# Performance work log

Hardware: AMD Instinct MI355X
Metric: run time of the kernel (lower is better)

## Reference

```python
import jax, jax.numpy as jnp
import numpy as np

B, D_IN, H = 8192, 4096, 128
E, N, C = 3, 256, 32          # experts, codebook_size, codebook_dim
D1, D2 = 512, 256             # down_units
U1, U2 = 256, 512             # up_units
CW = 0.25                     # commitment_weight


def setup_inputs() -> dict:
    key = jax.random.key(0)
    ks = jax.random.split(key, 16)
    s = 0.02
    f32 = jnp.float32
    inp = {
        'x':   jax.random.normal(ks[0], (B, D_IN), f32),
        # llm_down MLP: 4096 -> 512 -> 256 -> 128 (ReLU on hiddens, linear out)
        'Wd1': jax.random.normal(ks[1], (D_IN, D1), f32) * s, 'bd1': jnp.zeros((D1,), f32),
        'Wd2': jax.random.normal(ks[2], (D1, D2), f32) * s,  'bd2': jnp.zeros((D2,), f32),
        'Wd3': jax.random.normal(ks[3], (D2, H), f32) * s,   'bd3': jnp.zeros((H,), f32),
        # per-expert VQ: project_in 128->32, codebook [256,32], project_out 32->128
        'Win':  jax.random.normal(ks[4], (E, H, C), f32) * s, 'bin_': jnp.zeros((E, C), f32),
        'codebook': jax.random.normal(ks[5], (E, N, C), f32),
        'Wout': jax.random.normal(ks[6], (E, C, H), f32) * s, 'bout': jnp.zeros((E, H), f32),
        # llm_up MLP: 128 -> 256 -> 512 -> 4096
        'Wu1': jax.random.normal(ks[7], (H, U1), f32) * s,   'bu1': jnp.zeros((U1,), f32),
        'Wu2': jax.random.normal(ks[8], (U1, U2), f32) * s,  'bu2': jnp.zeros((U2,), f32),
        'Wu3': jax.random.normal(ks[9], (U2, D_IN), f32) * s, 'bu3': jnp.zeros((D_IN,), f32),
    }
    return inp


def _decorrelation_loss(qemb):
    # qemb: [B, E, H]
    b, e, h = qemb.shape
    cen = qemb - qemb.mean(axis=0, keepdims=True)
    cen = cen.transpose(1, 0, 2).reshape(e, -1)          # [E, B*H]
    cov = (cen @ cen.T) / (b * h - 1)                    # [E, E]
    std = jnp.sqrt(jnp.diag(cov))
    std = jnp.where(std > 1e-8, std, 1.0)
    corr = cov / jnp.outer(std, std)
    c2 = corr ** 2
    return c2.sum() - jnp.diag(c2).sum()


def _vq_experts(latent, Win, bin_, codebook, Wout, bout):
    # latent: [B,H]; all experts share the same (unmasked) latent.
    xe = jnp.einsum('bh,ehc->ebc', latent, Win) + bin_[:, None, :]      # [E,B,C]
    d2 = ((xe ** 2).sum(-1)[..., None]
          - 2.0 * jnp.einsum('ebc,enc->ebn', xe, codebook)
          + (codebook ** 2).sum(-1)[:, None, :])                        # [E,B,N]
    idx = jnp.argmin(d2, axis=-1)                                       # [E,B]
    q = jax.vmap(lambda c, i: c[i])(codebook, idx)                      # [E,B,C] gather
    commit = CW * jnp.mean((jax.lax.stop_gradient(q) - xe) ** 2, axis=(1, 2)).sum()
    quant = xe + jax.lax.stop_gradient(q - xe)                          # straight-through
    qe = jnp.einsum('ebc,ech->ebh', quant, Wout) + bout[:, None, :]     # [E,B,H]
    return qe, idx, commit


def reference(x, Wd1, bd1, Wd2, bd2, Wd3, bd3, Win, bin_, codebook, Wout, bout,
              Wu1, bu1, Wu2, bu2, Wu3, bu3):
    h = jax.nn.relu(x @ Wd1 + bd1)
    h = jax.nn.relu(h @ Wd2 + bd2)
    latent = h @ Wd3 + bd3                                              # [B,128]
    qe, idx, total_commit = _vq_experts(latent, Win, bin_, codebook, Wout, bout)
    qemb = qe.transpose(1, 0, 2)                                        # [B,E,H]
    decorr = _decorrelation_loss(qemb)
    rl = qemb.mean(axis=1)                                              # [B,H]
    u = jax.nn.relu(rl @ Wu1 + bu1)
    u = jax.nn.relu(u @ Wu2 + bu2)
    recon = jnp.clip(u @ Wu3 + bu3, -1.0, 1.0)                          # [B,4096]
    return (recon, idx.T, total_commit, decorr)
```

## Files before the change

kernel.cpp:

```cpp
#include <hip/hip_runtime.h>
#include <hip/hip_bf16.h>

using bf16 = __hip_bfloat16;

typedef __bf16 bf16x8 __attribute__((ext_vector_type(8)));
typedef float  f32x4  __attribute__((ext_vector_type(4)));
typedef unsigned int u32x4 __attribute__((ext_vector_type(4)));
typedef unsigned long long u64;
typedef unsigned short u16;
typedef unsigned int u32;

__device__ __forceinline__ float b2f(bf16 v) { return __bfloat162float(v); }
__device__ __forceinline__ bf16  f2b(float v) { return __float2bfloat16(v); }
__device__ __forceinline__ u16   bits(bf16 v) { return __builtin_bit_cast(u16, v); }

static constexpr size_t SZ_WD1S = 512ull  * 8192  * 2;
static constexpr size_t SZ_WD2S = 256ull  * 1536  * 2;
static constexpr size_t SZ_WFUS = 128ull  * 768   * 2;
static constexpr size_t SZ_WU1T = 256ull  * 128   * 2;
static constexpr size_t SZ_WU2T = 512ull  * 256   * 2;
static constexpr size_t SZ_WU3T = 4096ull * 512   * 2;
static constexpr size_t SZ_H1S  = 8192ull * 1536  * 2;
static constexpr size_t SZ_H2S  = 8192ull * 768   * 2;
static constexpr size_t SZ_XE   = 8192ull * 128   * 4;
static constexpr size_t SZ_QEMB = 3ull * 8192 * 128 * 4;
static constexpr size_t SZ_RL   = 8192ull * 128   * 2;
static constexpr size_t SZ_U1   = 8192ull * 256   * 2;
static constexpr size_t SZ_U2   = 8192ull * 512   * 2;
static constexpr size_t SZ_CNRM = 768ull * 4;
static constexpr size_t SZ_BFUS = 128ull * 4;
static constexpr size_t SZ_PART = 4ull * 8192 * 512 * 4;

static constexpr size_t OFF_WD1S = 0;
static constexpr size_t OFF_WD2S = OFF_WD1S + SZ_WD1S;
static constexpr size_t OFF_WFUS = OFF_WD2S + SZ_WD2S;
static constexpr size_t OFF_WU1T = OFF_WFUS + SZ_WFUS;
static constexpr size_t OFF_WU2T = OFF_WU1T + SZ_WU1T;
static constexpr size_t OFF_WU3T = OFF_WU2T + SZ_WU2T;
static constexpr size_t OFF_H1S  = OFF_WU3T + SZ_WU3T;
static constexpr size_t OFF_H2S  = OFF_H1S  + SZ_H1S;
static constexpr size_t OFF_XE   = OFF_H2S  + SZ_H2S;
static constexpr size_t OFF_QEMB = OFF_XE   + SZ_XE;
static constexpr size_t OFF_RL   = OFF_QEMB + SZ_QEMB;
static constexpr size_t OFF_U1   = OFF_RL   + SZ_RL;
static constexpr size_t OFF_U2   = OFF_U1   + SZ_U1;
static constexpr size_t OFF_CNRM = OFF_U2   + SZ_U2;
static constexpr size_t OFF_BFUS = OFF_CNRM + ((SZ_CNRM + 255) & ~size_t(255));
static constexpr size_t OFF_STAT = OFF_BFUS + ((SZ_BFUS + 255) & ~size_t(255));
static constexpr size_t OFF_PART = OFF_STAT + 2048;

__global__ void wtrans_bf16(const float* __restrict__ in, bf16* __restrict__ out,
                            int K, int N)
{
    __shared__ float tile[32][33];
    const int tx = threadIdx.x, ty = threadIdx.y;
    const int n0 = blockIdx.x * 32, k0 = blockIdx.y * 32;
    #pragma unroll
    for (int i = 0; i < 32; i += 8)
        tile[ty + i][tx] = in[(size_t)(k0 + ty + i) * N + n0 + tx];
    __syncthreads();
    #pragma unroll
    for (int i = 0; i < 32; i += 8)
        out[(size_t)(n0 + ty + i) * K + k0 + tx] = f2b(tile[tx][ty + i]);
}

__global__ void wtrans_split3(const float* __restrict__ in, bf16* __restrict__ out,
                              int K, int N)
{
    __shared__ float tile[32][33];
    const int tx = threadIdx.x, ty = threadIdx.y;
    const int n0 = blockIdx.x * 32, k0 = blockIdx.y * 32;
    #pragma unroll
    for (int i = 0; i < 32; i += 8)
        tile[ty + i][tx] = in[(size_t)(k0 + ty + i) * N + n0 + tx];
    __syncthreads();
    #pragma unroll
    for (int i = 0; i < 32; i += 8) {
        const float v = tile[tx][ty + i];
        const bf16 hi = f2b(v);
        const bf16 lo = f2b(v - b2f(hi));
        bf16* o = out + (size_t)(n0 + ty + i) * 3 * K + 3 * (k0 + tx);
        o[0] = hi; o[1] = lo; o[2] = hi;
    }
}

__global__ void wtrans_hilo(const float* __restrict__ in, bf16* __restrict__ out,
                            int K, int N)
{
    __shared__ float tile[32][33];
    const int tx = threadIdx.x, ty = threadIdx.y;
    const int n0 = blockIdx.x * 32, k0 = blockIdx.y * 32;
    #pragma unroll
    for (int i = 0; i < 32; i += 8)
        tile[ty + i][tx] = in[(size_t)(k0 + ty + i) * N + n0 + tx];
    __syncthreads();
    const int kg = k0 >> 5;
    #pragma unroll
    for (int i = 0; i < 32; i += 8) {
        const float v = tile[tx][ty + i];
        const bf16 hi = f2b(v);
        const bf16 lo = f2b(v - b2f(hi));
        bf16* o = out + (size_t)(n0 + ty + i) * 8192 + kg * 64 + tx;
        o[0] = hi; o[32] = lo;
    }
}

__global__ void cnorm_kernel(const float* __restrict__ cb, float* __restrict__ cnorm)
{
    const int i = blockIdx.x * blockDim.x + threadIdx.x;
    if (i < 768) {
        float s = 0.f;
        for (int k = 0; k < 32; ++k) { const float v = cb[i * 32 + k]; s += v * v; }
        cnorm[i] = s;
    }
}

__global__ __launch_bounds__(256)
void wfuse_kernel(const float* __restrict__ Wd3, const float* __restrict__ bd3,
                  const float* __restrict__ Win, const float* __restrict__ bin_,
                  bf16* __restrict__ BtS, float* __restrict__ bfuse)
{
    const int n = blockIdx.x;
    const int t = threadIdx.x;
    if (n >= 96) {
        bf16* o = BtS + (size_t)n * 768 + 3 * t;
        o[0] = f2b(0.f); o[1] = f2b(0.f); o[2] = f2b(0.f);
        if (t == 0) bfuse[n] = 0.f;
        return;
    }
    const int e = n >> 5, c = n & 31;
    float s = 0.f;
    for (int h = 0; h < 128; ++h)
        s += Wd3[t * 128 + h] * Win[(size_t)(e * 128 + h) * 32 + c];
    const bf16 hi = f2b(s);
    const bf16 lo = f2b(s - b2f(hi));
    bf16* o = BtS + (size_t)n * 768 + 3 * t;
    o[0] = hi; o[1] = lo; o[2] = hi;
    if (t == 0) {
        float b = bin_[e * 32 + c];
        for (int h = 0; h < 128; ++h)
            b += bd3[h] * Win[(size_t)(e * 128 + h) * 32 + c];
        bfuse[n] = b;
    }
}

__global__ __launch_bounds__(256, 4)
void gemm1_x3(const float* __restrict__ A, const bf16* __restrict__ Bhl,
              float* __restrict__ part)
{
    __shared__ bf16 As[128 * 64];
    __shared__ bf16 Bs[128 * 64];
    const int t = threadIdx.x, lane = t & 63, w = t >> 6;
    const int n0 = blockIdx.x * 128;
    const int m0 = blockIdx.y * 128;
    const int kz = blockIdx.z;
    const int wr = w >> 1, wc = w & 1, l15 = lane & 15, quad = lane >> 4;
    const int offh = ((quad ^ (l15 & 7)) << 3);
    const int offl = offh ^ 32;

    f32x4 acc[4][4];
    #pragma unroll
    for (int i = 0; i < 4; ++i)
        #pragma unroll
        for (int j = 0; j < 4; ++j)
            #pragma unroll
            for (int r = 0; r < 4; ++r) acc[i][j][r] = 0.f;

    const int arow = t >> 1, ahalf = t & 1, arx = arow & 7;
    bf16* const aw0 = As + arow * 64 + (((ahalf * 2 + 0) ^ arx) << 3);
    bf16* const aw1 = As + arow * 64 + (((ahalf * 2 + 1) ^ arx) << 3);
    bf16* const aw2 = As + arow * 64 + (((4 + ahalf * 2 + 0) ^ arx) << 3);
    bf16* const aw3 = As + arow * 64 + (((4 + ahalf * 2 + 1) ^ arx) << 3);

    int brow[4], bco[4];
    #pragma unroll
    for (int i = 0; i < 4; ++i) {
        const int p = i * 256 + t;
        brow[i] = p >> 3;
        bco[i] = ((p & 7) ^ (brow[i] & 7)) * 8;
    }

    const int s0 = kz * 32, s1 = s0 + 32;
    for (int ks = s0; ks < s1; ++ks) {
        const float* ap = A + (size_t)(m0 + arow) * 4096 + ks * 32 + ahalf * 16;
        float f[16];
        *(float4*)(f + 0)  = *(const float4*)(ap + 0);
        *(float4*)(f + 4)  = *(const float4*)(ap + 4);
        *(float4*)(f + 8)  = *(const float4*)(ap + 8);
        *(float4*)(f + 12) = *(const float4*)(ap + 12);
        #pragma unroll
        for (int i = 0; i < 4; ++i) {
            const bf16* gb = Bhl + (size_t)(n0 + brow[i]) * 8192 + ks * 64 + bco[i];
            __builtin_amdgcn_global_load_lds(
                (const __attribute__((address_space(1))) void*)gb,
                (__attribute__((address_space(3))) void*)(Bs + (size_t)(i * 256 + t) * 8), 16, 0, 0);
        }
        {
            u32x4 hv, lv;
            #pragma unroll
            for (int j = 0; j < 4; ++j) {
                const bf16 h0 = f2b(f[2 * j]), h1 = f2b(f[2 * j + 1]);
                const u32 l0 = bits(f2b(f[2 * j] - b2f(h0)));
                const u32 l1 = bits(f2b(f[2 * j + 1] - b2f(h1)));
                hv[j] = (u32)bits(h0) | ((u32)bits(h1) << 16);
                lv[j] = l0 | (l1 << 16);
            }
            *(u32x4*)aw0 = hv; *(u32x4*)aw2 = lv;
            #pragma unroll
            for (int j = 0; j < 4; ++j) {
                const bf16 h0 = f2b(f[8 + 2 * j]), h1 = f2b(f[8 + 2 * j + 1]);
                const u32 l0 = bits(f2b(f[8 + 2 * j] - b2f(h0)));
                const u32 l1 = bits(f2b(f[8 + 2 * j + 1] - b2f(h1)));
                hv[j] = (u32)bits(h0) | ((u32)bits(h1) << 16);
                lv[j] = l0 | (l1 << 16);
            }
            *(u32x4*)aw1 = hv; *(u32x4*)aw3 = lv;
        }
        __syncthreads();
        {
            bf16x8 ah[4], al[4];
            #pragma unroll
            for (int mi = 0; mi < 4; ++mi) {
                const bf16* ar = As + (wr * 64 + mi * 16 + l15) * 64;
                ah[mi] = *(const bf16x8*)(ar + offh);
                al[mi] = *(const bf16x8*)(ar + offl);
            }
            #pragma unroll
            for (int ni = 0; ni < 4; ++ni) {
                const bf16* br = Bs + (wc * 64 + ni * 16 + l15) * 64;
                const bf16x8 bh = *(const bf16x8*)(br + offh);
                const bf16x8 bl = *(const bf16x8*)(br + offl);
                #pragma unroll
                for (int mi = 0; mi < 4; ++mi) {
                    acc[mi][ni] = __builtin_amdgcn_mfma_f32_16x16x32_bf16(ah[mi], bh, acc[mi][ni], 0, 0, 0);
                    acc[mi][ni] = __builtin_amdgcn_mfma_f32_16x16x32_bf16(al[mi], bh, acc[mi][ni], 0, 0, 0);
                    acc[mi][ni] = __builtin_amdgcn_mfma_f32_16x16x32_bf16(ah[mi], bl, acc[mi][ni], 0, 0, 0);
                }
            }
        }
        __syncthreads();
    }

    float* op = part + (size_t)kz * (8192ull * 512);
    #pragma unroll
    for (int mi = 0; mi < 4; ++mi)
        #pragma unroll
        for (int ni = 0; ni < 4; ++ni) {
            const int col = n0 + wc * 64 + ni * 16 + l15;
            #pragma unroll
            for (int r = 0; r < 4; ++r) {
                const int row = m0 + wr * 64 + mi * 16 + quad * 4 + r;
                op[(size_t)row * 512 + col] = acc[mi][ni][r];
            }
        }
}

__global__ __launch_bounds__(256)
void h1_epi(const float* __restrict__ part, const float* __restrict__ bias,
            bf16* __restrict__ out)
{
    const int idx = blockIdx.x * 256 + threadIdx.x;
    const int r = idx >> 7, c4 = idx & 127;
    const size_t base = (size_t)r * 512 + c4 * 4;
    const float4 p0 = *(const float4*)(part + 0ull * 8192 * 512 + base);
    const float4 p1 = *(const float4*)(part + 1ull * 8192 * 512 + base);
    const float4 p2 = *(const float4*)(part + 2ull * 8192 * 512 + base);
    const float4 p3 = *(const float4*)(part + 3ull * 8192 * 512 + base);
    const float4 bv = *(const float4*)(bias + c4 * 4);
    float v[4];
    v[0] = p0.x + p1.x + p2.x + p3.x + bv.x;
    v[1] = p0.y + p1.y + p2.y + p3.y + bv.y;
    v[2] = p0.z + p1.z + p2.z + p3.z + bv.z;
    v[3] = p0.w + p1.w + p2.w + p3.w + bv.w;
    u64 h[4], l[4];
    #pragma unroll
    for (int j = 0; j < 4; ++j) {
        const float vv = v[j] > 0.f ? v[j] : 0.f;
        const bf16 hi = f2b(vv);
        h[j] = bits(hi);
        l[j] = bits(f2b(vv - b2f(hi)));
    }
    const u64 w0 = h[0] | (h[0] << 16) | (l[0] << 32) | (h[1] << 48);
    const u64 w1 = h[1] | (l[1] << 16) | (h[2] << 32) | (h[2] << 48);
    const u64 w2 = l[2] | (h[3] << 16) | (h[3] << 32) | (l[3] << 48);
    u64* dst = (u64*)(out + (size_t)r * 1536 + 12 * c4);
    dst[0] = w0; dst[1] = w1; dst[2] = w2;
}

template <int EPI, int RELU>
__global__ __launch_bounds__(256)
void gemm_bt(const bf16* __restrict__ A, const bf16* __restrict__ Bt,
             const float* __restrict__ bias, void* __restrict__ outp,
             int M, int N, int K)
{
    __shared__ bf16 As[128 * 64];
    __shared__ bf16 Bs[128 * 64];
    const int t = threadIdx.x, lane = t & 63, w = t >> 6;
    const int n0 = blockIdx.x * 128;
    const int m0 = blockIdx.y * 128;
    const int wr = w >> 1, wc = w & 1, l15 = lane & 15, quad = lane >> 4;
    const int l7 = l15 & 7;

    f32x4 acc[4][4];
    #pragma unroll
    for (int i = 0; i < 4; ++i)
        #pragma unroll
        for (int j = 0; j < 4; ++j)
            #pragma unroll
            for (int r = 0; r < 4; ++r) acc[i][j][r] = 0.f;

    int lrow[4], lcol[4];
    #pragma unroll
    for (int i = 0; i < 4; ++i) {
        const int c = i * 256 + t;
        lrow[i] = c >> 3;
        lcol[i] = ((c & 7) ^ (lrow[i] & 7)) * 8;
    }

    for (int k0 = 0; k0 < K; k0 += 64) {
        #pragma unroll
        for (int i = 0; i < 4; ++i) {
            const int c = i * 256 + t;
            const bf16* ga = A  + (size_t)(m0 + lrow[i]) * K + k0 + lcol[i];
            const bf16* gb = Bt + (size_t)(n0 + lrow[i]) * K + k0 + lcol[i];
            __builtin_amdgcn_global_load_lds(
                (const __attribute__((address_space(1))) void*)ga,
                (__attribute__((address_space(3))) void*)(As + (size_t)c * 8), 16, 0, 0);
            __builtin_amdgcn_global_load_lds(
                (const __attribute__((address_space(1))) void*)gb,
                (__attribute__((address_space(3))) void*)(Bs + (size_t)c * 8), 16, 0, 0);
        }
        __syncthreads();
        #pragma unroll
        for (int kk = 0; kk < 2; ++kk) {
            const int sw = (((kk << 2) | quad) ^ l7) << 3;
            bf16x8 af[4], bfr[4];
            #pragma unroll
            for (int mi = 0; mi < 4; ++mi)
                af[mi] = *(const bf16x8*)(As + (wr * 64 + mi * 16 + l15) * 64 + sw);
            #pragma unroll
            for (int ni = 0; ni < 4; ++ni)
                bfr[ni] = *(const bf16x8*)(Bs + (wc * 64 + ni * 16 + l15) * 64 + sw);
            #pragma unroll
            for (int mi = 0; mi < 4; ++mi)
                #pragma unroll
                for (int ni = 0; ni < 4; ++ni)
                    acc[mi][ni] = __builtin_amdgcn_mfma_f32_16x16x32_bf16(
                        af[mi], bfr[ni], acc[mi][ni], 0, 0, 0);
        }
        __syncthreads();
    }

    #pragma unroll
    for (int mi = 0; mi < 4; ++mi)
        #pragma unroll
        for (int ni = 0; ni < 4; ++ni) {
            const int col = n0 + wc * 64 + ni * 16 + l15;
            const float bv = bias[col];
            #pragma unroll
            for (int r = 0; r < 4; ++r) {
                const int row = m0 + wr * 64 + mi * 16 + quad * 4 + r;
                float v = acc[mi][ni][r] + bv;
                if (RELU) v = v > 0.f ? v : 0.f;
                if (EPI == 0) {
                    ((float*)outp)[(size_t)row * N + col] = v;
                } else if (EPI == 1) {
                    const bf16 hi = f2b(v);
                    const bf16 lo = f2b(v - b2f(hi));
                    bf16* o = (bf16*)outp + (size_t)row * 3 * N + 3 * col;
                    o[0] = hi; o[1] = hi; o[2] = lo;
                } else if (EPI == 2) {
                    ((bf16*)outp)[(size_t)row * N + col] = f2b(v);
                } else {
                    v = fminf(fmaxf(v, -1.f), 1.f);
                    ((float*)outp)[(size_t)row * N + col] = v;
                }
            }
        }
}

__global__ __launch_bounds__(256)
void vq2_kernel(const float* __restrict__ xe_buf, const float* __restrict__ cb,
                const float* __restrict__ cnorm, const float* __restrict__ Wout,
                const float* __restrict__ bout, float* __restrict__ qemb,
                float* __restrict__ idx_out, float* __restrict__ commit_acc)
{
    __shared__ float cb_s[256 * 36];
    __shared__ float wo_s[32 * 128];
    __shared__ float cn_s[256];
    __shared__ float bo_s[128];
    __shared__ float xe_s[4 * 32];
    __shared__ float q_s[4 * 32];
    __shared__ int   idx_s[4];
    __shared__ u64   wred[4][4];
    __shared__ float cred[256];

    const int e  = blockIdx.x >> 6;
    const int rb = blockIdx.x & 63;
    const int t = threadIdx.x, lane = t & 63, w = t >> 6;

    for (int j = t; j < 256 * 32; j += 256) {
        const int code = j >> 5, c = j & 31;
        cb_s[code * 36 + c] = cb[(size_t)e * 8192 + j];
    }
    for (int j = t; j < 4096; j += 256) wo_s[j] = Wout[(size_t)e * 4096 + j];
    cn_s[t] = cnorm[e * 256 + t];
    if (t < 128) bo_s[t] = bout[e * 128 + t];
    float commit_loc = 0.f;
    __syncthreads();

    for (int it = 0; it < 32; ++it) {
        const int r0 = rb * 128 + it * 4;
        if (t < 128) {
            const int r4 = t >> 5, c = t & 31;
            xe_s[r4 * 32 + c] = xe_buf[(size_t)(r0 + r4) * 128 + e * 32 + c];
        }
        __syncthreads();

        u64 key[4];
        {
            const float4* cp = (const float4*)(cb_s + t * 36);
            const float cn = cn_s[t];
            #pragma unroll
            for (int r4 = 0; r4 < 4; ++r4) {
                float dot = 0.f;
                #pragma unroll
                for (int c4 = 0; c4 < 8; ++c4) {
                    const float4 cv = cp[c4];
                    const float4 xv = *(const float4*)(xe_s + r4 * 32 + c4 * 4);
                    dot += xv.x * cv.x + xv.y * cv.y + xv.z * cv.z + xv.w * cv.w;
                }
                const float d = cn - 2.f * dot;
                u32 ub = __builtin_bit_cast(u32, d);
                ub = (ub & 0x80000000u) ? ~ub : (ub | 0x80000000u);
                key[r4] = ((u64)ub << 32) | (u32)t;
            }
        }
        #pragma unroll
        for (int off = 32; off; off >>= 1) {
            #pragma unroll
            for (int r4 = 0; r4 < 4; ++r4) {
                const u64 o = __shfl_down(key[r4], off, 64);
                if (o < key[r4]) key[r4] = o;
            }
        }
        if (lane == 0) {
            #pragma unroll
            for (int r4 = 0; r4 < 4; ++r4) wred[r4][w] = key[r4];
        }
        __syncthreads();
        if (t < 4) {
            u64 k = wred[t][0];
            #pragma unroll
            for (int ww = 1; ww < 4; ++ww) if (wred[t][ww] < k) k = wred[t][ww];
            const int code = (int)(k & 0xFFFFFFFFu);
            idx_s[t] = code;
            idx_out[(size_t)(r0 + t) * 3 + e] = (float)code;
        }
        __syncthreads();
        if (t < 128) {
            const int r4 = t >> 5, c = t & 31;
            const float q = cb_s[idx_s[r4] * 36 + c];
            q_s[r4 * 32 + c] = q;
            const float dd = q - xe_s[r4 * 32 + c];
            commit_loc += dd * dd;
        }
        __syncthreads();
        #pragma unroll
        for (int p = 0; p < 2; ++p) {
            const int j = p * 256 + t;
            const int r4 = j >> 7, h = j & 127;
            float s = bo_s[h];
            #pragma unroll
            for (int c = 0; c < 32; ++c) s += q_s[r4 * 32 + c] * wo_s[c * 128 + h];
            qemb[((size_t)e * 8192 + r0 + r4) * 128 + h] = s;
        }
        __syncthreads();
    }

    cred[t] = commit_loc;
    __syncthreads();
    for (int o = 128; o; o >>= 1) { if (t < o) cred[t] += cred[t + o]; __syncthreads(); }
    if (t == 0) atomicAdd(commit_acc, cred[0]);
}

__global__ __launch_bounds__(256)
void rlmean_kernel(const float* __restrict__ qemb, bf16* __restrict__ rl,
                   float* __restrict__ meanAcc)
{
    const int t = threadIdx.x, h = t & 127, half = t >> 7;
    const int r0 = blockIdx.x * 64;
    float a0 = 0.f, a1 = 0.f, a2 = 0.f;
    for (int r = r0 + half; r < r0 + 64; r += 2) {
        const float v0 = qemb[((size_t)0 * 8192 + r) * 128 + h];
        const float v1 = qemb[((size_t)1 * 8192 + r) * 128 + h];
        const float v2 = qemb[((size_t)2 * 8192 + r) * 128 + h];
        a0 += v0; a1 += v1; a2 += v2;
        rl[(size_t)r * 128 + h] = f2b((v0 + v1 + v2) * (1.f / 3.f));
    }
    __shared__ float red[3][256];
    red[0][t] = a0; red[1][t] = a1; red[2][t] = a2;
    __syncthreads();
    if (t < 128) {
        atomicAdd(&meanAcc[0 * 128 + h], red[0][t] + red[0][t + 128]);
        atomicAdd(&meanAcc[1 * 128 + h], red[1][t] + red[1][t + 128]);
        atomicAdd(&meanAcc[2 * 128 + h], red[2][t] + red[2][t + 128]);
    }
}

__global__ __launch_bounds__(256)
void gram_kernel(const float* __restrict__ qemb, const float* __restrict__ meanAcc,
                 double* __restrict__ gram)
{
    const int t = threadIdx.x;
    const int h = t & 127, half = t >> 7;
    const int b0 = blockIdx.x * 32;
    const float m0 = meanAcc[0 * 128 + h] * (1.f / 8192.f);
    const float m1 = meanAcc[1 * 128 + h] * (1.f / 8192.f);
    const float m2 = meanAcc[2 * 128 + h] * (1.f / 8192.f);
    float g[6] = {0, 0, 0, 0, 0, 0};
    for (int b = b0 + half; b < b0 + 32; b += 2) {
        const float v0 = qemb[((size_t)0 * 8192 + b) * 128 + h] - m0;
        const float v1 = qemb[((size_t)1 * 8192 + b) * 128 + h] - m1;
        const float v2 = qemb[((size_t)2 * 8192 + b) * 128 + h] - m2;
        g[0] += v0 * v0; g[1] += v0 * v1; g[2] += v0 * v2;
        g[3] += v1 * v1; g[4] += v1 * v2; g[5] += v2 * v2;
    }
    __shared__ float red[256];
    for (int i = 0; i < 6; ++i) {
        red[t] = g[i];
        __syncthreads();
        for (int o = 128; o; o >>= 1) { if (t < o) red[t] += red[t + o]; __syncthreads(); }
        if (t == 0) atomicAdd(&gram[i], (double)red[0]);
        __syncthreads();
    }
}

__global__ void final_kernel(const float* __restrict__ commit_acc,
                             const double* __restrict__ gram,
                             float* __restrict__ out2)
{
    if (threadIdx.x != 0 || blockIdx.x != 0) return;
    const double denom = 8192.0 * 128.0 - 1.0;
    const double c00 = gram[0] / denom, c01 = gram[1] / denom, c02 = gram[2] / denom;
    const double c11 = gram[3] / denom, c12 = gram[4] / denom, c22 = gram[5] / denom;
    double s0 = sqrt(c00), s1 = sqrt(c11), s2 = sqrt(c22);
    if (!(s0 > 1e-8)) s0 = 1.0;
    if (!(s1 > 1e-8)) s1 = 1.0;
    if (!(s2 > 1e-8)) s2 = 1.0;
    const double r01 = c01 / (s0 * s1), r02 = c02 / (s0 * s2), r12 = c12 / (s1 * s2);
    const double decorr = 2.0 * (r01 * r01 + r02 * r02 + r12 * r12);
    out2[0] = (float)((double)commit_acc[0] * (0.25 / (8192.0 * 32.0)));
    out2[1] = (float)decorr;
}

extern "C" void kernel_launch(void* const* d_in, const int* in_sizes, int n_in,
                              void* d_out, int out_size, void* d_ws, size_t ws_size,
                              hipStream_t stream)
{
    const float* x    = (const float*)d_in[0];
    const float* Wd1  = (const float*)d_in[1];
    const float* bd1  = (const float*)d_in[2];
    const float* Wd2  = (const float*)d_in[3];
    const float* bd2  = (const float*)d_in[4];
    const float* Wd3  = (const float*)d_in[5];
    const float* bd3  = (const float*)d_in[6];
    const float* Win  = (const float*)d_in[7];
    const float* bin_ = (const float*)d_in[8];
    const float* cb   = (const float*)d_in[9];
    const float* Wout = (const float*)d_in[10];
    const float* bout = (const float*)d_in[11];
    const float* Wu1  = (const float*)d_in[12];
    const float* bu1  = (const float*)d_in[13];
    const float* Wu2  = (const float*)d_in[14];
    const float* bu2  = (const float*)d_in[15];
    const float* Wu3  = (const float*)d_in[16];
    const float* bu3  = (const float*)d_in[17];

    char* ws = (char*)d_ws;
    bf16*  Wd1s   = (bf16*)(ws + OFF_WD1S);
    bf16*  Wd2s   = (bf16*)(ws + OFF_WD2S);
    bf16*  WfuseS = (bf16*)(ws + OFF_WFUS);
    bf16*  Wu1T   = (bf16*)(ws + OFF_WU1T);
    bf16*  Wu2T   = (bf16*)(ws + OFF_WU2T);
    bf16*  Wu3T   = (bf16*)(ws + OFF_WU3T);
    bf16*  h1s    = (bf16*)(ws + OFF_H1S);
    bf16*  h2s    = (bf16*)(ws + OFF_H2S);
    float* xe     = (float*)(ws + OFF_XE);
    float* qemb   = (float*)(ws + OFF_QEMB);
    bf16*  rl     = (bf16*)(ws + OFF_RL);
    bf16*  u1     = (bf16*)(ws + OFF_U1);
    bf16*  u2     = (bf16*)(ws + OFF_U2);
    float* cnorm  = (float*)(ws + OFF_CNRM);
    float* bfuse  = (float*)(ws + OFF_BFUS);
    float* commit = (float*)(ws + OFF_STAT);
    double* gram  = (double*)(ws + OFF_STAT + 8);
    float* meanA  = (float*)(ws + OFF_STAT + 64);
    float* part   = (float*)(ws + OFF_PART);

    float* out_f   = (float*)d_out;
    float* idx_out = out_f + (size_t)8192 * 4096;
    float* scal    = idx_out + (size_t)8192 * 3;

    hipMemsetAsync(ws + OFF_STAT, 0, 2048, stream);

    const dim3 tb(32, 8);
    wtrans_hilo<<<dim3(16, 128), tb, 0, stream>>>(Wd1, Wd1s, 4096, 512);
    wtrans_split3<<<dim3(8, 16),   tb, 0, stream>>>(Wd2, Wd2s, 512, 256);
    wtrans_bf16<<<dim3(8, 4),      tb, 0, stream>>>(Wu1, Wu1T, 128, 256);
    wtrans_bf16<<<dim3(16, 8),     tb, 0, stream>>>(Wu2, Wu2T, 256, 512);
    wtrans_bf16<<<dim3(128, 16),   tb, 0, stream>>>(Wu3, Wu3T, 512, 4096);
    cnorm_kernel<<<3, 256, 0, stream>>>(cb, cnorm);
    wfuse_kernel<<<128, 256, 0, stream>>>(Wd3, bd3, Win, bin_, WfuseS, bfuse);

    gemm1_x3<<<dim3(4, 64, 4), 256, 0, stream>>>(x, Wd1s, part);
    h1_epi<<<4096, 256, 0, stream>>>(part, bd1, h1s);
    gemm_bt<1, 1><<<dim3(2, 64), 256, 0, stream>>>(h1s, Wd2s, bd2, h2s, 8192, 256, 1536);
    gemm_bt<0, 0><<<dim3(1, 64), 256, 0, stream>>>(h2s, WfuseS, bfuse, xe, 8192, 128, 768);

    vq2_kernel<<<192, 256, 0, stream>>>(xe, cb, cnorm, Wout, bout, qemb, idx_out, commit);
    rlmean_kernel<<<128, 256, 0, stream>>>(qemb, rl, meanA);
    gram_kernel<<<256, 256, 0, stream>>>(qemb, meanA, gram);
    final_kernel<<<1, 64, 0, stream>>>(commit, gram, scal);

    gemm_bt<2, 1><<<dim3(2, 64),  256, 0, stream>>>(rl, Wu1T, bu1, u1,    8192, 256,  128);
    gemm_bt<2, 1><<<dim3(4, 64),  256, 0, stream>>>(u1, Wu2T, bu2, u2,    8192, 512,  256);
    gemm_bt<3, 0><<<dim3(32, 64), 256, 0, stream>>>(u2, Wu3T, bu3, out_f, 8192, 4096, 512);

    (void)in_sizes; (void)n_in; (void)out_size; (void)ws_size;
}
```

Measured before the change: 627.0 us.

## Remap gemm1 blocks per XCD and split VQ kernel into more blocks

The first GEMM's block index is remapped so that blocks landing on the same XCD (bid & 7) share the same N/K weight panel, which should improve L2 reuse of the B operand across the chiplets. Separately, the VQ kernel launches 768 blocks of 32 rows each instead of 192 blocks of 128 rows, so more CUs stay busy. The cost is that each VQ block reloads the codebook and Wout into shared memory over fewer rows, which raises redundant global traffic.

Measured after the change: 586.8 us. 1.07x faster.

```diff
diff --git a/kernel.cpp b/kernel.cpp
--- a/kernel.cpp
+++ b/kernel.cpp
@@ -151,9 +151,12 @@
     __shared__ bf16 As[128 * 64];
     __shared__ bf16 Bs[128 * 64];
     const int t = threadIdx.x, lane = t & 63, w = t >> 6;
-    const int n0 = blockIdx.x * 128;
-    const int m0 = blockIdx.y * 128;
-    const int kz = blockIdx.z;
+    const int bid = blockIdx.x + blockIdx.y * 4 + blockIdx.z * 256;
+    const int xcd = bid & 7, j = bid >> 3;
+    const int panel = xcd + 8 * (j >> 6);
+    const int n0 = (panel & 3) * 128;
+    const int kz = panel >> 2;
+    const int m0 = (j & 63) * 128;
     const int wr = w >> 1, wc = w & 1, l15 = lane & 15, quad = lane >> 4;
     const int offh = ((quad ^ (l15 & 7)) << 3);
     const int offl = offh ^ 32;
@@ -162,9 +165,9 @@
     #pragma unroll
     for (int i = 0; i < 4; ++i)
         #pragma unroll
-        for (int j = 0; j < 4; ++j)
-            #pragma unroll
-            for (int r = 0; r < 4; ++r) acc[i][j][r] = 0.f;
+        for (int jj = 0; jj < 4; ++jj)
+            #pragma unroll
+            for (int r = 0; r < 4; ++r) acc[i][jj][r] = 0.f;
 
     const int arow = t >> 1, ahalf = t & 1, arx = arow & 7;
     bf16* const aw0 = As + arow * 64 + (((ahalf * 2 + 0) ^ arx) << 3);
@@ -198,21 +201,21 @@
         {
             u32x4 hv, lv;
             #pragma unroll
-            for (int j = 0; j < 4; ++j) {
-                const bf16 h0 = f2b(f[2 * j]), h1 = f2b(f[2 * j + 1]);
-                const u32 l0 = bits(f2b(f[2 * j] - b2f(h0)));
-                const u32 l1 = bits(f2b(f[2 * j + 1] - b2f(h1)));
-                hv[j] = (u32)bits(h0) | ((u32)bits(h1) << 16);
-                lv[j] = l0 | (l1 << 16);
+            for (int jj = 0; jj < 4; ++jj) {
+                const bf16 h0 = f2b(f[2 * jj]), h1 = f2b(f[2 * jj + 1]);
+                const u32 l0 = bits(f2b(f[2 * jj] - b2f(h0)));
+                const u32 l1 = bits(f2b(f[2 * jj + 1] - b2f(h1)));
+                hv[jj] = (u32)bits(h0) | ((u32)bits(h1) << 16);
+                lv[jj] = l0 | (l1 << 16);
             }
             *(u32x4*)aw0 = hv; *(u32x4*)aw2 = lv;
             #pragma unroll
-            for (int j = 0; j < 4; ++j) {
-                const bf16 h0 = f2b(f[8 + 2 * j]), h1 = f2b(f[8 + 2 * j + 1]);
-                const u32 l0 = bits(f2b(f[8 + 2 * j] - b2f(h0)));
-                const u32 l1 = bits(f2b(f[8 + 2 * j + 1] - b2f(h1)));
-                hv[j] = (u32)bits(h0) | ((u32)bits(h1) << 16);
-                lv[j] = l0 | (l1 << 16);
+            for (int jj = 0; jj < 4; ++jj) {
+                const bf16 h0 = f2b(f[8 + 2 * jj]), h1 = f2b(f[8 + 2 * jj + 1]);
+                const u32 l0 = bits(f2b(f[8 + 2 * jj] - b2f(h0)));
+                const u32 l1 = bits(f2b(f[8 + 2 * jj + 1] - b2f(h1)));
+                hv[jj] = (u32)bits(h0) | ((u32)bits(h1) << 16);
+                lv[jj] = l0 | (l1 << 16);
             }
             *(u32x4*)aw1 = hv; *(u32x4*)aw3 = lv;
         }
@@ -395,8 +398,8 @@
     __shared__ u64   wred[4][4];
     __shared__ float cred[256];
 
-    const int e  = blockIdx.x >> 6;
-    const int rb = blockIdx.x & 63;
+    const int e  = blockIdx.x >> 8;
+    const int rb = blockIdx.x & 255;
     const int t = threadIdx.x, lane = t & 63, w = t >> 6;
 
     for (int j = t; j < 256 * 32; j += 256) {
@@ -409,8 +412,8 @@
     float commit_loc = 0.f;
     __syncthreads();
 
-    for (int it = 0; it < 32; ++it) {
-        const int r0 = rb * 128 + it * 4;
+    for (int it = 0; it < 8; ++it) {
+        const int r0 = rb * 32 + it * 4;
         if (t < 128) {
             const int r4 = t >> 5, c = t & 31;
             xe_s[r4 * 32 + c] = xe_buf[(size_t)(r0 + r4) * 128 + e * 32 + c];
@@ -618,7 +621,7 @@
     gemm_bt<1, 1><<<dim3(2, 64), 256, 0, stream>>>(h1s, Wd2s, bd2, h2s, 8192, 256, 1536);
     gemm_bt<0, 0><<<dim3(1, 64), 256, 0, stream>>>(h2s, WfuseS, bfuse, xe, 8192, 128, 768);
 
-    vq2_kernel<<<192, 256, 0, stream>>>(xe, cb, cnorm, Wout, bout, qemb, idx_out, commit);
+    vq2_kernel<<<768, 256, 0, stream>>>(xe, cb, cnorm, Wout, bout, qemb, idx_out, commit);
     rlmean_kernel<<<128, 256, 0, stream>>>(qemb, rl, meanA);
     gram_kernel<<<256, 256, 0, stream>>>(qemb, meanA, gram);
     final_kernel<<<1, 64, 0, stream>>>(commit, gram, scal);
```
